# Kernel tuning notes

Measured on AMD Instinct MI355X. Metric: run time of the kernel, lower is better.

The kernel has to match this reference:

```python
import math
import jax, jax.numpy as jnp
import numpy as np

H = 1024          # hidden size
NH = 16           # num attention heads
HD = H // NH      # head dim = 64
MAXPOS = 1024
HYP_W = 0.5


def setup_inputs() -> dict:
    key = jax.random.key(0)
    ks = jax.random.split(key, 9)
    B, S = 4, 1024
    scale = 1.0 / math.sqrt(H)
    return {
        "hidden_states": jax.random.normal(ks[0], (B, S, H), jnp.float32),
        "attention_mask": jnp.zeros((B, 1, 1, S), jnp.float32),
        "hyperbolic_attention_scores": jax.random.normal(ks[1], (B, S, S), jnp.float32),
        "Wq": jax.random.normal(ks[2], (H, H), jnp.float32) * scale,
        "bq": jnp.zeros((H,), jnp.float32),
        "Wk": jax.random.normal(ks[3], (H, H), jnp.float32) * scale,
        "bk": jnp.zeros((H,), jnp.float32),
        "Wv": jax.random.normal(ks[4], (H, H), jnp.float32) * scale,
        "bv": jnp.zeros((H,), jnp.float32),
        "dist_emb": jax.random.normal(ks[5], (2 * MAXPOS - 1, HD), jnp.float32) * 0.02,
    }


def reference(hidden_states, attention_mask, hyperbolic_attention_scores,
              Wq, bq, Wk, bk, Wv, bv, dist_emb):
    B, S, _ = hidden_states.shape

    def split_heads(x):  # [B,S,H] -> [B,NH,S,HD]
        return x.reshape(B, S, NH, HD).transpose(0, 2, 1, 3)

    q = split_heads(hidden_states @ Wq + bq)
    k = split_heads(hidden_states @ Wk + bk)
    v = split_heads(hidden_states @ Wv + bv)

    # raw scores [B,NH,Sq,Sk]
    scores = jnp.einsum("bhqd,bhkd->bhqk", q, k)

    # relative_key_query position bias
    distance = jnp.arange(S)[:, None] - jnp.arange(S)[None, :]  # [Sq,Sk]
    pe = dist_emb[distance + MAXPOS - 1]                        # [Sq,Sk,HD]
    scores = scores + jnp.einsum("bhld,lrd->bhlr", q, pe)
    scores = scores + jnp.einsum("bhrd,lrd->bhlr", k, pe)

    scores = scores / math.sqrt(HD)
    scores = scores + HYP_W * hyperbolic_attention_scores[:, None, :, :]
    scores = scores + attention_mask

    probs = jax.nn.softmax(scores, axis=-1)
    ctx = jnp.einsum("bhqk,bhkd->bhqd", probs, v)  # [B,NH,S,HD]
    ctx = ctx.transpose(0, 2, 1, 3).reshape(B, S, H)
    return ctx
```

## Files before the change

### kernel.cpp

```cpp
#include <hip/hip_runtime.h>
#include <math.h>

#define S_SEQ 1024
#define NHEAD 16
#define HDIM  64
#define BATCH 4

typedef __attribute__((ext_vector_type(8))) short bf16x8;
typedef __attribute__((ext_vector_type(4))) float f32x4;

__device__ __forceinline__ float bf2f(unsigned short h) {
    union { unsigned u; float f; } un; un.u = ((unsigned)h) << 16; return un.f;
}
__device__ __forceinline__ unsigned short f2bf(float x) {
    union { float f; unsigned u; } un; un.f = x;
    unsigned r = un.u + 0x7FFFu + ((un.u >> 16) & 1u);
    return (unsigned short)(r >> 16);
}
__device__ __forceinline__ unsigned pack2bf(float a, float b) {
    return (unsigned)f2bf(a) | ((unsigned)f2bf(b) << 16);
}
__device__ __forceinline__ void glds16(const unsigned short* g, unsigned short* l) {
    __builtin_amdgcn_global_load_lds(
        (const __attribute__((address_space(1))) void*)g,
        (__attribute__((address_space(3))) void*)l, 16, 0, 0);
}

#define HS_F4 1048576
#define PE_F4 32752
__global__ __launch_bounds__(256) void conv_kernel(
    const float* __restrict__ hs, const float* __restrict__ de,
    unsigned short* __restrict__ hsb, unsigned short* __restrict__ peb)
{
    int i = blockIdx.x * 256 + threadIdx.x;
    if (i < HS_F4) {
        float4 v = ((const float4*)hs)[i];
        uint2 o;
        o.x = pack2bf(v.x, v.y);
        o.y = pack2bf(v.z, v.w);
        *(uint2*)(hsb + 4 * (size_t)i) = o;
    } else if (i < HS_F4 + PE_F4) {
        int j = i - HS_F4;
        float4 v = ((const float4*)de)[j];
        uint2 o;
        o.x = pack2bf(v.x, v.y);
        o.y = pack2bf(v.z, v.w);
        *(uint2*)(peb + 4 * (size_t)j) = o;
    }
}

__global__ __launch_bounds__(256) void wtrans_kernel(
    const float* __restrict__ Wq, const float* __restrict__ Wk,
    const float* __restrict__ Wv, unsigned short* __restrict__ wt)
{
    __shared__ float tl[64 * 67];
    const int which = blockIdx.z;
    const float* W = (which == 0) ? Wq : (which == 1) ? Wk : Wv;
    unsigned short* out = wt + (size_t)which * 1024 * 1024;
    const int k0 = blockIdx.x * 64, n0 = blockIdx.y * 64;
    const int t = threadIdx.x;

#pragma unroll
    for (int it = 0; it < 4; ++it) {
        int idx = t + it * 256;
        int kr = idx >> 4;
        int c4 = (idx & 15) << 2;
        float4 v = *(const float4*)(W + (size_t)(k0 + kr) * 1024 + n0 + c4);
        tl[kr * 67 + c4 + 0] = v.x; tl[kr * 67 + c4 + 1] = v.y;
        tl[kr * 67 + c4 + 2] = v.z; tl[kr * 67 + c4 + 3] = v.w;
    }
    __syncthreads();
#pragma unroll
    for (int it = 0; it < 2; ++it) {
        int idx = t + it * 256;
        int nr = idx >> 3;
        int k8 = (idx & 7) << 3;
        unsigned short r[8];
#pragma unroll
        for (int e = 0; e < 8; ++e) r[e] = f2bf(tl[(k8 + e) * 67 + nr]);
        uint4 o;
        o.x = (unsigned)r[0] | ((unsigned)r[1] << 16);
        o.y = (unsigned)r[2] | ((unsigned)r[3] << 16);
        o.z = (unsigned)r[4] | ((unsigned)r[5] << 16);
        o.w = (unsigned)r[6] | ((unsigned)r[7] << 16);
        *(uint4*)(out + (size_t)(n0 + nr) * 1024 + k0 + k8) = o;
    }
}

__global__ __launch_bounds__(256, 3) void qkv_mfma_kernel(
    const unsigned short* __restrict__ hsb, const unsigned short* __restrict__ wt,
    const float* __restrict__ bq, const float* __restrict__ bk,
    const float* __restrict__ bv,
    unsigned short* __restrict__ qo, unsigned short* __restrict__ ko,
    unsigned short* __restrict__ vo)
{
    __shared__ unsigned short As[128 * 64];
    __shared__ unsigned short Bs[128 * 64];

    const int t = threadIdx.x;
    const int lane = t & 63, w = t >> 6;
    const int l16 = lane & 15, quad = lane >> 4;
    const int wm = w >> 1, wn = w & 1;
    const int lrow = lane >> 3, cs = lane & 7;
    const int n0 = blockIdx.x * 128, m0 = blockIdx.y * 128;
    const int which = blockIdx.z;
    const unsigned short* wts = wt + (size_t)which * 1024 * 1024;
    const float* bias = (which == 0) ? bq : (which == 1) ? bk : bv;

    f32x4 acc[4][4];
#pragma unroll
    for (int i = 0; i < 4; ++i)
#pragma unroll
        for (int j = 0; j < 4; ++j) acc[i][j] = (f32x4){0.f, 0.f, 0.f, 0.f};

    for (int kk = 0; kk < 1024; kk += 64) {
#pragma unroll
        for (int it = 0; it < 4; ++it) {
            int mrow = 32 * w + 8 * it + lrow;
            int kch = cs ^ (mrow & 7);
            glds16(hsb + (size_t)(m0 + mrow) * 1024 + kk + kch * 8,
                   &As[(32 * w + 8 * it) * 64]);
            glds16(wts + (size_t)(n0 + mrow) * 1024 + kk + kch * 8,
                   &Bs[(32 * w + 8 * it) * 64]);
        }
        __syncthreads();

        bf16x8 af[4][2], bf[4][2];
#pragma unroll
        for (int i = 0; i < 4; ++i) {
            int am = 64 * wm + 16 * i + l16;
            int base = am * 64;
            af[i][0] = *(bf16x8*)&As[base + ((quad ^ (am & 7)) << 3)];
            af[i][1] = *(bf16x8*)&As[base + (((quad + 4) ^ (am & 7)) << 3)];
        }
#pragma unroll
        for (int j = 0; j < 4; ++j) {
            int bn = 64 * wn + 16 * j + l16;
            int base = bn * 64;
            bf[j][0] = *(bf16x8*)&Bs[base + ((quad ^ (bn & 7)) << 3)];
            bf[j][1] = *(bf16x8*)&Bs[base + (((quad + 4) ^ (bn & 7)) << 3)];
        }
#pragma unroll
        for (int i = 0; i < 4; ++i)
#pragma unroll
            for (int j = 0; j < 4; ++j) {
                acc[i][j] = __builtin_amdgcn_mfma_f32_16x16x32_bf16(
                    af[i][0], bf[j][0], acc[i][j], 0, 0, 0);
                acc[i][j] = __builtin_amdgcn_mfma_f32_16x16x32_bf16(
                    af[i][1], bf[j][1], acc[i][j], 0, 0, 0);
            }
        __syncthreads();
    }

#pragma unroll
    for (int j = 0; j < 4; ++j) {
        int n = n0 + 64 * wn + 16 * j + l16;
        float bvv = bias[n];
        int hh = n >> 6, hd = n & 63;
#pragma unroll
        for (int i = 0; i < 4; ++i) {
            int mb = m0 + 64 * wm + 16 * i + 4 * quad;
            int bb = mb >> 10, s = mb & 1023;
            if (which == 2) {
                uint2 o;
                o.x = pack2bf(acc[i][j][0] + bvv, acc[i][j][1] + bvv);
                o.y = pack2bf(acc[i][j][2] + bvv, acc[i][j][3] + bvv);
                *(uint2*)(vo + ((size_t)(bb * NHEAD + hh) * HDIM + hd) * S_SEQ + s) = o;
            } else {
                unsigned short* out = (which == 0) ? qo : ko;
#pragma unroll
                for (int r = 0; r < 4; ++r)
                    out[((size_t)(bb * NHEAD + hh) * S_SEQ + s + r) * HDIM + hd] =
                        f2bf(acc[i][j][r] + bvv);
            }
        }
    }
}

__global__ __launch_bounds__(256, 3) void attn_mfma_kernel(
    const unsigned short* __restrict__ qw, const unsigned short* __restrict__ kw,
    const unsigned short* __restrict__ vtw, const unsigned short* __restrict__ peb,
    const float* __restrict__ hyp, const float* __restrict__ mask,
    float* __restrict__ out)
{
    __shared__ unsigned short ks[32 * 72];
    __shared__ unsigned short vT[64 * 40];
    __shared__ unsigned short pes[96 * 72];
    __shared__ unsigned short QDs[96 * 66];
    __shared__ unsigned short KDs[96 * 38];
    __shared__ unsigned short ps[64 * 40];

    const int t = threadIdx.x;
    const int lane = t & 63, w = t >> 6;
    const int l16 = lane & 15, quad = lane >> 4;
    const int l0 = blockIdx.x * 64;
    const int h = blockIdx.y, b = blockIdx.z;

    const unsigned short* qb = qw + ((size_t)(b * NHEAD + h) * S_SEQ + l0) * HDIM;
    const unsigned short* kb = kw + (size_t)(b * NHEAD + h) * S_SEQ * HDIM;
    const unsigned short* vtb = vtw + (size_t)(b * NHEAD + h) * HDIM * S_SEQ;
    const float* hypb = hyp + (size_t)b * S_SEQ * S_SEQ;
    const float* maskb = mask + b * S_SEQ;

    const bf16x8 qf0 = *(const bf16x8*)(qb + (16 * w + l16) * 64 + quad * 8);
    const bf16x8 qf1 = *(const bf16x8*)(qb + (16 * w + l16) * 64 + 32 + quad * 8);

    const int pb0 = l0 + 992;

#pragma unroll
    for (int it = 0; it < 2; ++it) {
        int idx = t + it * 256;
        int row = idx >> 3, c8 = (idx & 7) << 3;
        int ar = pb0 + 32 + row;
        int slot = ar % 96;
        int src = ar > 2046 ? 2046 : ar;
        *(uint4*)&pes[slot * 72 + c8] = *(const uint4*)(peb + (size_t)src * 64 + c8);
    }
    __syncthreads();
#pragma unroll
    for (int jd = 0; jd < 4; ++jd) {
        int slot = (pb0 + 32 + 16 * jd + l16) % 96;
        bf16x8 p0 = *(bf16x8*)&pes[slot * 72 + quad * 8];
        bf16x8 p1 = *(bf16x8*)&pes[slot * 72 + 32 + quad * 8];
        f32x4 aq = (f32x4){0.f, 0.f, 0.f, 0.f};
        aq = __builtin_amdgcn_mfma_f32_16x16x32_bf16(qf0, p0, aq, 0, 0, 0);
        aq = __builtin_amdgcn_mfma_f32_16x16x32_bf16(qf1, p1, aq, 0, 0, 0);
        int ad = slot * 66 + 16 * w + 4 * quad;
        *(unsigned*)&QDs[ad] = pack2bf(aq[0], aq[1]);
        *(unsigned*)&QDs[ad + 2] = pack2bf(aq[2], aq[3]);
    }

    f32x4 accO[4];
#pragma unroll
    for (int j = 0; j < 4; ++j) accO[j] = (f32x4){0.f, 0.f, 0.f, 0.f};
    float m_run[4], lsum[4];
#pragma unroll
    for (int i = 0; i < 4; ++i) { m_run[i] = -INFINITY; lsum[i] = 0.f; }

    int sb = pb0 % 96;

    for (int kt = 0; kt < 32; ++kt) {
        const int r0 = 32 * kt;
        const int pb = pb0 - r0;

        {
            int row = t >> 3, c8 = (t & 7) << 3;
            *(uint4*)&ks[row * 72 + c8] =
                *(const uint4*)(kb + (size_t)(r0 + row) * 64 + c8);
            int d = t >> 2, rc = (t & 3) << 3;
            *(uint4*)&vT[d * 40 + rc] =
                *(const uint4*)(vtb + (size_t)d * 1024 + r0 + rc);
            int slot = sb + row; if (slot >= 96) slot -= 96;
            *(uint4*)&pes[slot * 72 + c8] =
                *(const uint4*)(peb + (size_t)(pb + row) * 64 + c8);
        }
        __syncthreads();

        bf16x8 kfA0 = *(bf16x8*)&ks[(16 * (w & 1) + l16) * 72 + quad * 8];
        bf16x8 kfA1 = *(bf16x8*)&ks[(16 * (w & 1) + l16) * 72 + 32 + quad * 8];
        f32x4 accS[2];
#pragma unroll
        for (int j = 0; j < 2; ++j) {
            bf16x8 b0 = *(bf16x8*)&ks[(16 * j + l16) * 72 + quad * 8];
            bf16x8 b1 = *(bf16x8*)&ks[(16 * j + l16) * 72 + 32 + quad * 8];
            f32x4 a = (f32x4){0.f, 0.f, 0.f, 0.f};
            a = __builtin_amdgcn_mfma_f32_16x16x32_bf16(qf0, b0, a, 0, 0, 0);
            a = __builtin_amdgcn_mfma_f32_16x16x32_bf16(qf1, b1, a, 0, 0, 0);
            accS[j] = a;
        }
#pragma unroll
        for (int jd = 0; jd < 2; ++jd) {
            int slot = sb + 16 * jd + l16; if (slot >= 96) slot -= 96;
            bf16x8 p0 = *(bf16x8*)&pes[slot * 72 + quad * 8];
            bf16x8 p1 = *(bf16x8*)&pes[slot * 72 + 32 + quad * 8];
            f32x4 aq = (f32x4){0.f, 0.f, 0.f, 0.f};
            aq = __builtin_amdgcn_mfma_f32_16x16x32_bf16(qf0, p0, aq, 0, 0, 0);
            aq = __builtin_amdgcn_mfma_f32_16x16x32_bf16(qf1, p1, aq, 0, 0, 0);
            int ad = slot * 66 + 16 * w + 4 * quad;
            *(unsigned*)&QDs[ad] = pack2bf(aq[0], aq[1]);
            *(unsigned*)&QDs[ad + 2] = pack2bf(aq[2], aq[3]);
        }
#pragma unroll
        for (int jk = 0; jk < 3; ++jk) {
            int dd = 48 * (w >> 1) + 16 * jk + l16;
            int slot = sb + dd; if (slot >= 96) slot -= 96;
            bf16x8 p0 = *(bf16x8*)&pes[slot * 72 + quad * 8];
            bf16x8 p1 = *(bf16x8*)&pes[slot * 72 + 32 + quad * 8];
            f32x4 ak = (f32x4){0.f, 0.f, 0.f, 0.f};
            ak = __builtin_amdgcn_mfma_f32_16x16x32_bf16(kfA0, p0, ak, 0, 0, 0);
            ak = __builtin_amdgcn_mfma_f32_16x16x32_bf16(kfA1, p1, ak, 0, 0, 0);
            int ad = dd * 38 + 16 * (w & 1) + 4 * quad;
            *(unsigned*)&KDs[ad] = pack2bf(ak[0], ak[1]);
            *(unsigned*)&KDs[ad + 2] = pack2bf(ak[2], ak[3]);
        }
        __syncthreads();

        float sc[4][2], al[4];
#pragma unroll
        for (int j = 0; j < 2; ++j) {
            int r_loc = 16 * j + l16;
            float mv = maskb[r0 + r_loc];
#pragma unroll
            for (int i = 0; i < 4; ++i) {
                int ll = 16 * w + 4 * quad + i;
                int di = ll - r_loc + 31;
                int sl = sb + di; if (sl >= 96) sl -= 96;
                float qd = bf2f(QDs[sl * 66 + ll]);
                float kd = bf2f(KDs[di * 38 + r_loc]);
                float hv = hypb[(size_t)(l0 + ll) * 1024 + r0 + r_loc];
                sc[i][j] = (accS[j][i] + qd + kd) * 0.125f + 0.5f * hv + mv;
            }
        }
#pragma unroll
        for (int i = 0; i < 4; ++i) {
            float mx = fmaxf(sc[i][0], sc[i][1]);
#pragma unroll
            for (int off = 1; off < 16; off <<= 1)
                mx = fmaxf(mx, __shfl_xor(mx, off));
            float m_new = fmaxf(m_run[i], mx);
            al[i] = __expf(m_run[i] - m_new);
            float p0 = __expf(sc[i][0] - m_new);
            float p1 = __expf(sc[i][1] - m_new);
            sc[i][0] = p0; sc[i][1] = p1;
            float rs = p0 + p1;
#pragma unroll
            for (int off = 1; off < 16; off <<= 1)
                rs += __shfl_xor(rs, off);
            lsum[i] = lsum[i] * al[i] + rs;
            m_run[i] = m_new;
        }
#pragma unroll
        for (int i = 0; i < 4; ++i) {
            int ll = 16 * w + 4 * quad + i;
            ps[ll * 40 + l16] = f2bf(sc[i][0]);
            ps[ll * 40 + 16 + l16] = f2bf(sc[i][1]);
        }

        bf16x8 pf = *(bf16x8*)&ps[(16 * w + l16) * 40 + quad * 8];
#pragma unroll
        for (int jf = 0; jf < 4; ++jf) {
            bf16x8 vv = *(bf16x8*)&vT[(16 * jf + l16) * 40 + quad * 8];
            f32x4 o = accO[jf];
#pragma unroll
            for (int r = 0; r < 4; ++r) o[r] *= al[r];
            o = __builtin_amdgcn_mfma_f32_16x16x32_bf16(pf, vv, o, 0, 0, 0);
            accO[jf] = o;
        }
        sb -= 32; if (sb < 0) sb += 96;
        __syncthreads();
    }

#pragma unroll
    for (int jf = 0; jf < 4; ++jf)
#pragma unroll
        for (int i = 0; i < 4; ++i) {
            int ll = 16 * w + 4 * quad + i;
            out[((size_t)b * S_SEQ + l0 + ll) * 1024 + h * 64 + 16 * jf + l16] =
                accO[jf][i] / lsum[i];
        }
}

extern "C" void kernel_launch(void* const* d_in, const int* in_sizes, int n_in,
                              void* d_out, int out_size, void* d_ws, size_t ws_size,
                              hipStream_t stream) {
    const float* hs   = (const float*)d_in[0];
    const float* mask = (const float*)d_in[1];
    const float* hyp  = (const float*)d_in[2];
    const float* Wq   = (const float*)d_in[3];
    const float* bq   = (const float*)d_in[4];
    const float* Wk   = (const float*)d_in[5];
    const float* bk   = (const float*)d_in[6];
    const float* Wv   = (const float*)d_in[7];
    const float* bv   = (const float*)d_in[8];
    const float* de   = (const float*)d_in[9];

    char* ws = (char*)d_ws;
    unsigned short* qw  = (unsigned short*)(ws);
    unsigned short* kw  = (unsigned short*)(ws + (8u << 20));
    unsigned short* vtw = (unsigned short*)(ws + (16u << 20));
    unsigned short* hsb = (unsigned short*)(ws + (24u << 20));
    unsigned short* wt  = (unsigned short*)(ws + (32u << 20));
    unsigned short* peb = (unsigned short*)(ws + (38u << 20));

    conv_kernel<<<dim3((HS_F4 + PE_F4 + 255) / 256), 256, 0, stream>>>(hs, de, hsb, peb);
    wtrans_kernel<<<dim3(16, 16, 3), 256, 0, stream>>>(Wq, Wk, Wv, wt);
    qkv_mfma_kernel<<<dim3(8, 32, 3), 256, 0, stream>>>(hsb, wt, bq, bk, bv, qw, kw, vtw);
    attn_mfma_kernel<<<dim3(16, NHEAD, BATCH), 256, 0, stream>>>(
        qw, kw, vtw, peb, hyp, mask, (float*)d_out);
}
```

Before: 284.3 us.

## Transpose score MFMAs, load K/V fragments from global, swizzle LDS, single barrier

Restructures the attention kernel's inner loop. S^T is computed by swapping the MFMA operands so each lane owns one query row, which turns the softmax reductions into two cross-quad shuffles. K and V fragments are now loaded straight from global memory into registers, with K and the positional-embedding rows prefetched for the next tile, so the K/V LDS staging and one barrier per iteration go away. LDS tiles use XOR swizzles, hyp and mask are read as float4, and KD work is rebalanced across the four waves. Occupancy is raised to 4 blocks per CU, which adds register pressure and more redundant global loads that rely on L2 hits.

```diff
diff --git a/kernel.cpp b/kernel.cpp
--- a/kernel.cpp
+++ b/kernel.cpp
@@ -8,6 +8,8 @@
 
 typedef __attribute__((ext_vector_type(8))) short bf16x8;
 typedef __attribute__((ext_vector_type(4))) float f32x4;
+
+#define MFMA16 __builtin_amdgcn_mfma_f32_16x16x32_bf16
 
 __device__ __forceinline__ float bf2f(unsigned short h) {
     union { unsigned u; float f; } un; un.u = ((unsigned)h) << 16; return un.f;
@@ -144,10 +146,8 @@
         for (int i = 0; i < 4; ++i)
 #pragma unroll
             for (int j = 0; j < 4; ++j) {
-                acc[i][j] = __builtin_amdgcn_mfma_f32_16x16x32_bf16(
-                    af[i][0], bf[j][0], acc[i][j], 0, 0, 0);
-                acc[i][j] = __builtin_amdgcn_mfma_f32_16x16x32_bf16(
-                    af[i][1], bf[j][1], acc[i][j], 0, 0, 0);
+                acc[i][j] = MFMA16(af[i][0], bf[j][0], acc[i][j], 0, 0, 0);
+                acc[i][j] = MFMA16(af[i][1], bf[j][1], acc[i][j], 0, 0, 0);
             }
         __syncthreads();
     }
@@ -177,187 +177,251 @@
     }
 }
 
-__global__ __launch_bounds__(256, 3) void attn_mfma_kernel(
+__global__ __launch_bounds__(256, 4) void attn_mfma_kernel(
     const unsigned short* __restrict__ qw, const unsigned short* __restrict__ kw,
     const unsigned short* __restrict__ vtw, const unsigned short* __restrict__ peb,
     const float* __restrict__ hyp, const float* __restrict__ mask,
     float* __restrict__ out)
 {
-    __shared__ unsigned short ks[32 * 72];
-    __shared__ unsigned short vT[64 * 40];
-    __shared__ unsigned short pes[96 * 72];
-    __shared__ unsigned short QDs[96 * 66];
-    __shared__ unsigned short KDs[96 * 38];
-    __shared__ unsigned short ps[64 * 40];
+    __shared__ unsigned short pes[96 * 64];
+    __shared__ unsigned short QDs[64 * 100];
+    __shared__ unsigned short KDs[96 * 36];
+    __shared__ unsigned short ps[64 * 32];
 
     const int t = threadIdx.x;
     const int lane = t & 63, w = t >> 6;
     const int l16 = lane & 15, quad = lane >> 4;
+    const int lL = 16 * w + l16;
     const int l0 = blockIdx.x * 64;
     const int h = blockIdx.y, b = blockIdx.z;
 
     const unsigned short* qb = qw + ((size_t)(b * NHEAD + h) * S_SEQ + l0) * HDIM;
     const unsigned short* kb = kw + (size_t)(b * NHEAD + h) * S_SEQ * HDIM;
     const unsigned short* vtb = vtw + (size_t)(b * NHEAD + h) * HDIM * S_SEQ;
-    const float* hypb = hyp + (size_t)b * S_SEQ * S_SEQ;
+    const float* hypb = hyp + (size_t)b * S_SEQ * S_SEQ + (size_t)(l0 + lL) * S_SEQ;
     const float* maskb = mask + b * S_SEQ;
 
-    const bf16x8 qf0 = *(const bf16x8*)(qb + (16 * w + l16) * 64 + quad * 8);
-    const bf16x8 qf1 = *(const bf16x8*)(qb + (16 * w + l16) * 64 + 32 + quad * 8);
+    const bf16x8 qf0 = *(const bf16x8*)(qb + lL * 64 + quad * 8);
+    const bf16x8 qf1 = *(const bf16x8*)(qb + lL * 64 + 32 + quad * 8);
 
     const int pb0 = l0 + 992;
+    int sb = pb0 % 96;
+    int cQ = (pb0 - lL) % 96;
+
+    const int strow = t >> 3, stp = t & 7;
+    const int swzl = (lL >> 1) & 3;
+
+    f32x4 accO[4];
+#pragma unroll
+    for (int jf = 0; jf < 4; ++jf) accO[jf] = (f32x4){0.f, 0.f, 0.f, 0.f};
+    float m_run = -INFINITY, lsum = 0.f;
 
 #pragma unroll
     for (int it = 0; it < 2; ++it) {
         int idx = t + it * 256;
-        int row = idx >> 3, c8 = (idx & 7) << 3;
+        int row = idx >> 3, p = idx & 7;
         int ar = pb0 + 32 + row;
         int slot = ar % 96;
         int src = ar > 2046 ? 2046 : ar;
-        *(uint4*)&pes[slot * 72 + c8] = *(const uint4*)(peb + (size_t)src * 64 + c8);
+        *(uint4*)&pes[slot * 64 + (p << 3)] =
+            *(const uint4*)(peb + (size_t)src * 64 + ((p ^ (slot & 7)) << 3));
     }
     __syncthreads();
+
 #pragma unroll
     for (int jd = 0; jd < 4; ++jd) {
-        int slot = (pb0 + 32 + 16 * jd + l16) % 96;
-        bf16x8 p0 = *(bf16x8*)&pes[slot * 72 + quad * 8];
-        bf16x8 p1 = *(bf16x8*)&pes[slot * 72 + 32 + quad * 8];
+        int s = sb + 32 + 16 * jd + l16; if (s >= 96) s -= 96;
+        const int sw = s & 7;
+        bf16x8 p0 = *(bf16x8*)&pes[s * 64 + ((quad ^ sw) << 3)];
+        bf16x8 p1 = *(bf16x8*)&pes[s * 64 + (((quad + 4) ^ sw) << 3)];
         f32x4 aq = (f32x4){0.f, 0.f, 0.f, 0.f};
-        aq = __builtin_amdgcn_mfma_f32_16x16x32_bf16(qf0, p0, aq, 0, 0, 0);
-        aq = __builtin_amdgcn_mfma_f32_16x16x32_bf16(qf1, p1, aq, 0, 0, 0);
-        int ad = slot * 66 + 16 * w + 4 * quad;
-        *(unsigned*)&QDs[ad] = pack2bf(aq[0], aq[1]);
-        *(unsigned*)&QDs[ad + 2] = pack2bf(aq[2], aq[3]);
-    }
-
-    f32x4 accO[4];
-#pragma unroll
-    for (int j = 0; j < 4; ++j) accO[j] = (f32x4){0.f, 0.f, 0.f, 0.f};
-    float m_run[4], lsum[4];
-#pragma unroll
-    for (int i = 0; i < 4; ++i) { m_run[i] = -INFINITY; lsum[i] = 0.f; }
-
-    int sb = pb0 % 96;
+        aq = MFMA16(p0, qf0, aq, 0, 0, 0);
+        aq = MFMA16(p1, qf1, aq, 0, 0, 0);
+        int cb = cQ + 32 + 16 * jd + 4 * quad;
+#pragma unroll
+        for (int i = 0; i < 4; ++i) {
+            int c = cb + i; if (c >= 96) c -= 96;
+            QDs[lL * 100 + c] = f2bf(aq[i]);
+        }
+    }
+
+    bf16x8 kf00 = *(const bf16x8*)(kb + (size_t)l16 * 64 + quad * 8);
+    bf16x8 kf01 = *(const bf16x8*)(kb + (size_t)l16 * 64 + 32 + quad * 8);
+    bf16x8 kf10 = *(const bf16x8*)(kb + (size_t)(16 + l16) * 64 + quad * 8);
+    bf16x8 kf11 = *(const bf16x8*)(kb + (size_t)(16 + l16) * 64 + 32 + quad * 8);
+    uint4 peReg;
+    {
+        int slot = sb + strow; if (slot >= 96) slot -= 96;
+        peReg = *(const uint4*)(peb + (size_t)(pb0 + strow) * 64 +
+                                ((stp ^ (slot & 7)) << 3));
+    }
+
+    const int fstart = (w < 2) ? 3 * w : 2 * w + 2;
+    const int fcnt   = (w < 2) ? 3 : 2;
 
     for (int kt = 0; kt < 32; ++kt) {
         const int r0 = 32 * kt;
-        const int pb = pb0 - r0;
+
+        const float4 hv0 = *(const float4*)(hypb + r0 + 4 * quad);
+        const float4 hv1 = *(const float4*)(hypb + r0 + 16 + 4 * quad);
+        const float4 mv0 = *(const float4*)(maskb + r0 + 4 * quad);
+        const float4 mv1 = *(const float4*)(maskb + r0 + 16 + 4 * quad);
 
         {
-            int row = t >> 3, c8 = (t & 7) << 3;
-            *(uint4*)&ks[row * 72 + c8] =
-                *(const uint4*)(kb + (size_t)(r0 + row) * 64 + c8);
-            int d = t >> 2, rc = (t & 3) << 3;
-            *(uint4*)&vT[d * 40 + rc] =
-                *(const uint4*)(vtb + (size_t)d * 1024 + r0 + rc);
-            int slot = sb + row; if (slot >= 96) slot -= 96;
-            *(uint4*)&pes[slot * 72 + c8] =
-                *(const uint4*)(peb + (size_t)(pb + row) * 64 + c8);
+            int slot = sb + strow; if (slot >= 96) slot -= 96;
+            *(uint4*)&pes[slot * 64 + (stp << 3)] = peReg;
         }
         __syncthreads();
 
-        bf16x8 kfA0 = *(bf16x8*)&ks[(16 * (w & 1) + l16) * 72 + quad * 8];
-        bf16x8 kfA1 = *(bf16x8*)&ks[(16 * (w & 1) + l16) * 72 + 32 + quad * 8];
-        f32x4 accS[2];
-#pragma unroll
-        for (int j = 0; j < 2; ++j) {
-            bf16x8 b0 = *(bf16x8*)&ks[(16 * j + l16) * 72 + quad * 8];
-            bf16x8 b1 = *(bf16x8*)&ks[(16 * j + l16) * 72 + 32 + quad * 8];
-            f32x4 a = (f32x4){0.f, 0.f, 0.f, 0.f};
-            a = __builtin_amdgcn_mfma_f32_16x16x32_bf16(qf0, b0, a, 0, 0, 0);
-            a = __builtin_amdgcn_mfma_f32_16x16x32_bf16(qf1, b1, a, 0, 0, 0);
-            accS[j] = a;
-        }
+        f32x4 accS0 = (f32x4){0.f, 0.f, 0.f, 0.f};
+        f32x4 accS1 = (f32x4){0.f, 0.f, 0.f, 0.f};
+        accS0 = MFMA16(kf00, qf0, accS0, 0, 0, 0);
+        accS0 = MFMA16(kf01, qf1, accS0, 0, 0, 0);
+        accS1 = MFMA16(kf10, qf0, accS1, 0, 0, 0);
+        accS1 = MFMA16(kf11, qf1, accS1, 0, 0, 0);
+
 #pragma unroll
         for (int jd = 0; jd < 2; ++jd) {
-            int slot = sb + 16 * jd + l16; if (slot >= 96) slot -= 96;
-            bf16x8 p0 = *(bf16x8*)&pes[slot * 72 + quad * 8];
-            bf16x8 p1 = *(bf16x8*)&pes[slot * 72 + 32 + quad * 8];
+            int s = sb + 16 * jd + l16; if (s >= 96) s -= 96;
+            const int sw = s & 7;
+            bf16x8 p0 = *(bf16x8*)&pes[s * 64 + ((quad ^ sw) << 3)];
+            bf16x8 p1 = *(bf16x8*)&pes[s * 64 + (((quad + 4) ^ sw) << 3)];
             f32x4 aq = (f32x4){0.f, 0.f, 0.f, 0.f};
-            aq = __builtin_amdgcn_mfma_f32_16x16x32_bf16(qf0, p0, aq, 0, 0, 0);
-            aq = __builtin_amdgcn_mfma_f32_16x16x32_bf16(qf1, p1, aq, 0, 0, 0);
-            int ad = slot * 66 + 16 * w + 4 * quad;
-            *(unsigned*)&QDs[ad] = pack2bf(aq[0], aq[1]);
-            *(unsigned*)&QDs[ad + 2] = pack2bf(aq[2], aq[3]);
-        }
+            aq = MFMA16(p0, qf0, aq, 0, 0, 0);
+            aq = MFMA16(p1, qf1, aq, 0, 0, 0);
+            int cb = cQ + 16 * jd + 4 * quad;
+#pragma unroll
+            for (int i = 0; i < 4; ++i) {
+                int c = cb + i; if (c >= 96) c -= 96;
+                QDs[lL * 100 + c] = f2bf(aq[i]);
+            }
+        }
+
 #pragma unroll
         for (int jk = 0; jk < 3; ++jk) {
-            int dd = 48 * (w >> 1) + 16 * jk + l16;
-            int slot = sb + dd; if (slot >= 96) slot -= 96;
-            bf16x8 p0 = *(bf16x8*)&pes[slot * 72 + quad * 8];
-            bf16x8 p1 = *(bf16x8*)&pes[slot * 72 + 32 + quad * 8];
-            f32x4 ak = (f32x4){0.f, 0.f, 0.f, 0.f};
-            ak = __builtin_amdgcn_mfma_f32_16x16x32_bf16(kfA0, p0, ak, 0, 0, 0);
-            ak = __builtin_amdgcn_mfma_f32_16x16x32_bf16(kfA1, p1, ak, 0, 0, 0);
-            int ad = dd * 38 + 16 * (w & 1) + 4 * quad;
-            *(unsigned*)&KDs[ad] = pack2bf(ak[0], ak[1]);
-            *(unsigned*)&KDs[ad + 2] = pack2bf(ak[2], ak[3]);
+            if (jk < fcnt) {
+                const int f = fstart + jk;
+                const int diB = 16 * ((f + 1) >> 1);
+                const int rB = (f & 1) ? 0 : 16;
+                int s = sb + diB + l16; if (s >= 96) s -= 96;
+                const int sw = s & 7;
+                bf16x8 p0 = *(bf16x8*)&pes[s * 64 + ((quad ^ sw) << 3)];
+                bf16x8 p1 = *(bf16x8*)&pes[s * 64 + (((quad + 4) ^ sw) << 3)];
+                f32x4 ak = (f32x4){0.f, 0.f, 0.f, 0.f};
+                if (rB == 0) {
+                    ak = MFMA16(p0, kf00, ak, 0, 0, 0);
+                    ak = MFMA16(p1, kf01, ak, 0, 0, 0);
+                } else {
+                    ak = MFMA16(p0, kf10, ak, 0, 0, 0);
+                    ak = MFMA16(p1, kf11, ak, 0, 0, 0);
+                }
+                const int colr = rB + l16;
+                const int aB = diB + colr + 4 * quad - 16;
+#pragma unroll
+                for (int i = 0; i < 4; ++i)
+                    KDs[(aB + i) * 36 + colr] = f2bf(ak[i]);
+            }
         }
         __syncthreads();
 
-        float sc[4][2], al[4];
-#pragma unroll
-        for (int j = 0; j < 2; ++j) {
-            int r_loc = 16 * j + l16;
-            float mv = maskb[r0 + r_loc];
-#pragma unroll
-            for (int i = 0; i < 4; ++i) {
-                int ll = 16 * w + 4 * quad + i;
-                int di = ll - r_loc + 31;
-                int sl = sb + di; if (sl >= 96) sl -= 96;
-                float qd = bf2f(QDs[sl * 66 + ll]);
-                float kd = bf2f(KDs[di * 38 + r_loc]);
-                float hv = hypb[(size_t)(l0 + ll) * 1024 + r0 + r_loc];
-                sc[i][j] = (accS[j][i] + qd + kd) * 0.125f + 0.5f * hv + mv;
-            }
-        }
-#pragma unroll
-        for (int i = 0; i < 4; ++i) {
-            float mx = fmaxf(sc[i][0], sc[i][1]);
-#pragma unroll
-            for (int off = 1; off < 16; off <<= 1)
-                mx = fmaxf(mx, __shfl_xor(mx, off));
-            float m_new = fmaxf(m_run[i], mx);
-            al[i] = __expf(m_run[i] - m_new);
-            float p0 = __expf(sc[i][0] - m_new);
-            float p1 = __expf(sc[i][1] - m_new);
-            sc[i][0] = p0; sc[i][1] = p1;
-            float rs = p0 + p1;
-#pragma unroll
-            for (int off = 1; off < 16; off <<= 1)
-                rs += __shfl_xor(rs, off);
-            lsum[i] = lsum[i] * al[i] + rs;
-            m_run[i] = m_new;
-        }
-#pragma unroll
-        for (int i = 0; i < 4; ++i) {
-            int ll = 16 * w + 4 * quad + i;
-            ps[ll * 40 + l16] = f2bf(sc[i][0]);
-            ps[ll * 40 + 16 + l16] = f2bf(sc[i][1]);
-        }
-
-        bf16x8 pf = *(bf16x8*)&ps[(16 * w + l16) * 40 + quad * 8];
+        {
+            const int r0n = (kt < 31) ? r0 + 32 : r0;
+            kf00 = *(const bf16x8*)(kb + (size_t)(r0n + l16) * 64 + quad * 8);
+            kf01 = *(const bf16x8*)(kb + (size_t)(r0n + l16) * 64 + 32 + quad * 8);
+            kf10 = *(const bf16x8*)(kb + (size_t)(r0n + 16 + l16) * 64 + quad * 8);
+            kf11 = *(const bf16x8*)(kb + (size_t)(r0n + 16 + l16) * 64 + 32 + quad * 8);
+            int sbn = sb, pbn = pb0 - r0n;
+            if (kt < 31) { sbn = sb - 32; if (sbn < 0) sbn += 96; }
+            int slotN = sbn + strow; if (slotN >= 96) slotN -= 96;
+            peReg = *(const uint4*)(peb + (size_t)(pbn + strow) * 64 +
+                                    ((stp ^ (slotN & 7)) << 3));
+        }
+        bf16x8 vvA[4];
+#pragma unroll
+        for (int jf = 0; jf < 4; ++jf)
+            vvA[jf] = *(const bf16x8*)(vtb + (size_t)(16 * jf + l16) * S_SEQ +
+                                       r0 + quad * 8);
+
+        float sc0[4], sc1[4];
+        {
+            uint2 qd2 = *(uint2*)&QDs[lL * 100 + sb + 28 - 4 * quad];
+            uint2 kd2 = *(uint2*)&KDs[(lL + 15) * 36 + 4 * quad];
+            sc0[0] = (accS0[0] + bf2f((unsigned short)(qd2.y >> 16)) +
+                      bf2f((unsigned short)(kd2.x & 0xffff))) * 0.125f + 0.5f * hv0.x + mv0.x;
+            sc0[1] = (accS0[1] + bf2f((unsigned short)(qd2.y & 0xffff)) +
+                      bf2f((unsigned short)(kd2.x >> 16))) * 0.125f + 0.5f * hv0.y + mv0.y;
+            sc0[2] = (accS0[2] + bf2f((unsigned short)(qd2.x >> 16)) +
+                      bf2f((unsigned short)(kd2.y & 0xffff))) * 0.125f + 0.5f * hv0.z + mv0.z;
+            sc0[3] = (accS0[3] + bf2f((unsigned short)(qd2.x & 0xffff)) +
+                      bf2f((unsigned short)(kd2.y >> 16))) * 0.125f + 0.5f * hv0.w + mv0.w;
+        }
+        {
+            uint2 qd2 = *(uint2*)&QDs[lL * 100 + sb + 12 - 4 * quad];
+            uint2 kd2 = *(uint2*)&KDs[(lL + 15) * 36 + 16 + 4 * quad];
+            sc1[0] = (accS1[0] + bf2f((unsigned short)(qd2.y >> 16)) +
+                      bf2f((unsigned short)(kd2.x & 0xffff))) * 0.125f + 0.5f * hv1.x + mv1.x;
+            sc1[1] = (accS1[1] + bf2f((unsigned short)(qd2.y & 0xffff)) +
+                      bf2f((unsigned short)(kd2.x >> 16))) * 0.125f + 0.5f * hv1.y + mv1.y;
+            sc1[2] = (accS1[2] + bf2f((unsigned short)(qd2.x >> 16)) +
+                      bf2f((unsigned short)(kd2.y & 0xffff))) * 0.125f + 0.5f * hv1.z + mv1.z;
+            sc1[3] = (accS1[3] + bf2f((unsigned short)(qd2.x & 0xffff)) +
+                      bf2f((unsigned short)(kd2.y >> 16))) * 0.125f + 0.5f * hv1.w + mv1.w;
+        }
+
+        float mx = fmaxf(fmaxf(fmaxf(sc0[0], sc0[1]), fmaxf(sc0[2], sc0[3])),
+                         fmaxf(fmaxf(sc1[0], sc1[1]), fmaxf(sc1[2], sc1[3])));
+        mx = fmaxf(mx, __shfl_xor(mx, 16));
+        mx = fmaxf(mx, __shfl_xor(mx, 32));
+        const float m_new = fmaxf(m_run, mx);
+        const float al = __expf(m_run - m_new);
+        m_run = m_new;
+        float rs = 0.f;
+#pragma unroll
+        for (int i = 0; i < 4; ++i) { sc0[i] = __expf(sc0[i] - m_new); rs += sc0[i]; }
+#pragma unroll
+        for (int i = 0; i < 4; ++i) { sc1[i] = __expf(sc1[i] - m_new); rs += sc1[i]; }
+        rs += __shfl_xor(rs, 16);
+        rs += __shfl_xor(rs, 32);
+        lsum = lsum * al + rs;
+
+        {
+            uint2 pw;
+            pw.x = pack2bf(sc0[0], sc0[1]); pw.y = pack2bf(sc0[2], sc0[3]);
+            *(uint2*)&ps[lL * 32 + (((quad >> 1) ^ swzl) << 3) + 4 * (quad & 1)] = pw;
+            pw.x = pack2bf(sc1[0], sc1[1]); pw.y = pack2bf(sc1[2], sc1[3]);
+            *(uint2*)&ps[lL * 32 + (((2 + (quad >> 1)) ^ swzl) << 3) + 4 * (quad & 1)] = pw;
+        }
+
+        const bf16x8 pf = *(const bf16x8*)&ps[lL * 32 + ((quad ^ swzl) << 3)];
+        const float alv0 = __shfl(al, 4 * quad + 0);
+        const float alv1 = __shfl(al, 4 * quad + 1);
+        const float alv2 = __shfl(al, 4 * quad + 2);
+        const float alv3 = __shfl(al, 4 * quad + 3);
 #pragma unroll
         for (int jf = 0; jf < 4; ++jf) {
-            bf16x8 vv = *(bf16x8*)&vT[(16 * jf + l16) * 40 + quad * 8];
             f32x4 o = accO[jf];
-#pragma unroll
-            for (int r = 0; r < 4; ++r) o[r] *= al[r];
-            o = __builtin_amdgcn_mfma_f32_16x16x32_bf16(pf, vv, o, 0, 0, 0);
+            o[0] *= alv0; o[1] *= alv1; o[2] *= alv2; o[3] *= alv3;
+            o = MFMA16(pf, vvA[jf], o, 0, 0, 0);
             accO[jf] = o;
         }
+
         sb -= 32; if (sb < 0) sb += 96;
-        __syncthreads();
-    }
-
-#pragma unroll
-    for (int jf = 0; jf < 4; ++jf)
-#pragma unroll
-        for (int i = 0; i < 4; ++i) {
-            int ll = 16 * w + 4 * quad + i;
-            out[((size_t)b * S_SEQ + l0 + ll) * 1024 + h * 64 + 16 * jf + l16] =
-                accO[jf][i] / lsum[i];
-        }
+        cQ -= 32; if (cQ < 0) cQ += 96;
+    }
+
+    const float ls0 = __shfl(lsum, 4 * quad + 0);
+    const float ls1 = __shfl(lsum, 4 * quad + 1);
+    const float ls2 = __shfl(lsum, 4 * quad + 2);
+    const float ls3 = __shfl(lsum, 4 * quad + 3);
+#pragma unroll
+    for (int jf = 0; jf < 4; ++jf) {
+        const size_t col = (size_t)h * 64 + 16 * jf + l16;
+        float* ob = out + ((size_t)b * S_SEQ + l0 + 16 * w + 4 * quad) * 1024 + col;
+        ob[0]        = accO[jf][0] / ls0;
+        ob[1024]     = accO[jf][1] / ls1;
+        ob[2048]     = accO[jf][2] / ls2;
+        ob[3072]     = accO[jf][3] / ls3;
+    }
 }
 
 extern "C" void kernel_launch(void* const* d_in, const int* in_sizes, int n_in,
```

After: 298.0 us. 1.05x slower.
